# Optimization experiments

Hardware: AMD Instinct MI355X
Metric: run time of the kernel (lower is better)

## Reference

```python
import jax, jax.numpy as jnp
import numpy as np

D_MODEL = 1024
NUM_HEADS = 16
HEAD_DIM = D_MODEL // NUM_HEADS


def setup_inputs() -> dict:
    key = jax.random.key(0)
    ks = jax.random.split(key, 11)
    S, B, D = 2048, 2, D_MODEL
    scale = 1.0 / np.sqrt(D)
    inp = {
        'query': jax.random.normal(ks[0], (S, B, D), dtype=jnp.float32),
        'key': jax.random.normal(ks[1], (S, B, D), dtype=jnp.float32),
        'value': jax.random.normal(ks[2], (S, B, D), dtype=jnp.float32),
        'Wq': jax.random.normal(ks[3], (D, D), dtype=jnp.float32) * scale,
        'bq': jnp.zeros((D,), dtype=jnp.float32),
        'Wk': jax.random.normal(ks[4], (D, D), dtype=jnp.float32) * scale,
        'bk': jnp.zeros((D,), dtype=jnp.float32),
        'Wv': jax.random.normal(ks[5], (D, D), dtype=jnp.float32) * scale,
        'bv': jnp.zeros((D,), dtype=jnp.float32),
        'Wo': jax.random.normal(ks[6], (D, D), dtype=jnp.float32) * scale,
        'bo': jnp.zeros((D,), dtype=jnp.float32),
    }
    return inp


def reference(query, key, value, Wq, bq, Wk, bk, Wv, bv, Wo, bo):
    # query/key/value: [S, B, D] (seq-first, as in the torch module)
    S, B, D = query.shape
    H, Hd = NUM_HEADS, HEAD_DIM
    # Linear: x @ W.T + b (torch convention), then split heads -> [B, H, S, Hd]
    def proj_heads(x, W, b):
        y = jnp.einsum('sbd,ed->sbe', x, W) + b  # [S, B, D]
        return y.reshape(x.shape[0], B, H, Hd).transpose(1, 2, 0, 3)
    q = proj_heads(query, Wq, bq)   # [B, H, S, Hd]
    k = proj_heads(key, Wk, bk)     # [B, H, Sk, Hd]
    v = proj_heads(value, Wv, bv)   # [B, H, Sk, Hd]
    scores = jnp.einsum('bhsd,bhtd->bhst', q, k) / jnp.sqrt(jnp.asarray(Hd, q.dtype))
    probs = jax.nn.softmax(scores, axis=-1)  # dropout p=0.0 -> identity
    attn = jnp.einsum('bhst,bhtd->bhsd', probs, v)  # [B, H, S, Hd]
    attn = attn.transpose(2, 0, 1, 3).reshape(S, B, D)  # [S, B, D]
    out = jnp.einsum('sbd,ed->sbe', attn, Wo) + bo
    return out
```

## Files before the change

### kernel.cpp

```cpp
#include <hip/hip_runtime.h>
#include <stdint.h>

#define S_LEN 2048
#define BATCH 2
#define DM    1024
#define NH    16
#define HD    64
#define MROWS 4096

typedef float f32x4 __attribute__((ext_vector_type(4)));
typedef short bfrag __attribute__((ext_vector_type(8)));
typedef unsigned short u16x4_t __attribute__((ext_vector_type(4)));
typedef unsigned short u16x8_t __attribute__((ext_vector_type(8)));
typedef int i32x4_t __attribute__((ext_vector_type(4)));

#define EXP2F(x) __builtin_amdgcn_exp2f(x)

__device__ inline f32x4 mfma16(bfrag a, bfrag b, f32x4 c) {
    return __builtin_amdgcn_mfma_f32_16x16x32_bf16(a, b, c, 0, 0, 0);
}

__device__ inline unsigned short bf16_rn(float x) {
    unsigned u = __builtin_bit_cast(unsigned, x);
    return (unsigned short)((u + 0x7fffu + ((u >> 16) & 1u)) >> 16);
}

__device__ inline void split_bf16(float x, unsigned short &h, unsigned short &l) {
    unsigned u = __builtin_bit_cast(unsigned, x);
    h = (unsigned short)(u >> 16);
    float hf = __builtin_bit_cast(float, u & 0xffff0000u);
    float r = x - hf;
    l = (unsigned short)(__builtin_bit_cast(unsigned, r) >> 16);
}

__device__ inline unsigned pack_rhu(float a, float b) {
    unsigned ua = __builtin_bit_cast(unsigned, a) + 0x8000u;
    unsigned ub = __builtin_bit_cast(unsigned, b) + 0x8000u;
    return (ua >> 16) | (ub & 0xffff0000u);
}

typedef __attribute__((address_space(1))) const unsigned int as1_u32;
typedef __attribute__((address_space(3))) unsigned int as3_u32;
__device__ inline void async16(void* lds, const void* g) {
    __builtin_amdgcn_global_load_lds((as1_u32*)g, (as3_u32*)lds, 16, 0, 0);
}

__global__ __launch_bounds__(256)
void cvt_kernel(const float* __restrict__ Wq, const float* __restrict__ Wk,
                const float* __restrict__ Wv, const float* __restrict__ Wo,
                const float* __restrict__ Qin, const float* __restrict__ Kin,
                const float* __restrict__ Vin,
                unsigned short* __restrict__ Wqb, unsigned short* __restrict__ Wkb,
                unsigned short* __restrict__ Wvb,
                unsigned short* __restrict__ Woh, unsigned short* __restrict__ Wol,
                unsigned short* __restrict__ Qa,  unsigned short* __restrict__ Ka,
                unsigned short* __restrict__ Va)
{
    const int z = blockIdx.z;
    size_t idx = ((size_t)blockIdx.x * 256 + threadIdx.x) * 8;
    const size_t limit = (z < 4) ? (size_t)DM * DM : (size_t)MROWS * DM;
    if (idx >= limit) return;
    const float* src = (z == 0) ? Wq : (z == 1) ? Wk : (z == 2) ? Wv :
                       (z == 3) ? Wo : (z == 4) ? Qin : (z == 5) ? Kin : Vin;
    float4 f0 = *(const float4*)&src[idx];
    float4 f1 = *(const float4*)&src[idx + 4];
    if (z != 3) {
        unsigned short* dst = (z == 0) ? Wqb : (z == 1) ? Wkb : (z == 2) ? Wvb :
                              (z == 4) ? Qa  : (z == 5) ? Ka  : Va;
        u16x8_t v = { bf16_rn(f0.x), bf16_rn(f0.y), bf16_rn(f0.z), bf16_rn(f0.w),
                      bf16_rn(f1.x), bf16_rn(f1.y), bf16_rn(f1.z), bf16_rn(f1.w) };
        *(u16x8_t*)&dst[idx] = v;
    } else {
        unsigned short h0,h1,h2,h3,h4,h5,h6,h7, l0,l1,l2,l3,l4,l5,l6,l7;
        split_bf16(f0.x,h0,l0); split_bf16(f0.y,h1,l1);
        split_bf16(f0.z,h2,l2); split_bf16(f0.w,h3,l3);
        split_bf16(f1.x,h4,l4); split_bf16(f1.y,h5,l5);
        split_bf16(f1.z,h6,l6); split_bf16(f1.w,h7,l7);
        u16x8_t vh = {h0,h1,h2,h3,h4,h5,h6,h7};
        u16x8_t vl = {l0,l1,l2,l3,l4,l5,l6,l7};
        *(u16x8_t*)&Woh[idx] = vh;
        *(u16x8_t*)&Wol[idx] = vl;
    }
}

__global__ __launch_bounds__(256)
void qkv_gemm(const unsigned short* __restrict__ Qa,
              const unsigned short* __restrict__ Ka,
              const unsigned short* __restrict__ Va,
              const unsigned short* __restrict__ Wqb,
              const unsigned short* __restrict__ Wkb,
              const unsigned short* __restrict__ Wvb,
              const float* __restrict__ bq, const float* __restrict__ bk,
              const float* __restrict__ bv,
              unsigned short* __restrict__ Qb, unsigned short* __restrict__ Kb,
              unsigned short* __restrict__ Vt)
{
    __shared__ unsigned short sA[128*32];
    __shared__ unsigned short sB[128*32];

    const int tid = threadIdx.x, lane = tid & 63, w4 = tid >> 6;
    const int m16 = lane & 15, q4 = lane >> 4;
    const int wr = w4 >> 1, wc = w4 & 1;
    const int z = blockIdx.z;

    int id = blockIdx.x + 8 * blockIdx.y;
    int j  = id >> 3;
    const int m0 = ((id & 7) * 4 + (j & 3)) * 128;
    const int n0 = (j >> 2) * 128;

    const unsigned short* A = (z == 0) ? Qa : (z == 1) ? Ka : Va;
    const unsigned short* W = (z == 0) ? Wqb : (z == 1) ? Wkb : Wvb;
    const float* bias = (z == 0) ? bq : (z == 1) ? bk : bv;
    unsigned short* outp = (z == 0) ? Qb : (z == 1) ? Kb : Vt;

    const int G1 = tid + 256;
    const int r0 = tid >> 2, g0 = (tid & 3) ^ ((r0 ^ (r0 >> 2)) & 3);
    const int r1 = G1  >> 2, g1 = (G1  & 3) ^ ((r1 ^ (r1 >> 2)) & 3);
    const char* gA0 = (const char*)A + (size_t)(m0 + r0) * 2048 + g0 * 16;
    const char* gA1 = (const char*)A + (size_t)(m0 + r1) * 2048 + g1 * 16;
    const char* gB0 = (const char*)W + (size_t)(n0 + r0) * 2048 + g0 * 16;
    const char* gB1 = (const char*)W + (size_t)(n0 + r1) * 2048 + g1 * 16;
    char* ldsA0 = (char*)sA + w4 * 1024;
    char* ldsA1 = (char*)sA + 4096 + w4 * 1024;
    char* ldsB0 = (char*)sB + w4 * 1024;
    char* ldsB1 = (char*)sB + 4096 + w4 * 1024;

    int offA[4], offB[4];
    #pragma unroll
    for (int rt = 0; rt < 4; rt++) {
        int r = wr * 64 + rt * 16 + m16;
        offA[rt] = r * 32 + ((q4 ^ ((r ^ (r >> 2)) & 3)) << 3);
    }
    #pragma unroll
    for (int ct = 0; ct < 4; ct++) {
        int r = wc * 64 + ct * 16 + m16;
        offB[ct] = r * 32 + ((q4 ^ ((r ^ (r >> 2)) & 3)) << 3);
    }

    f32x4 acc[4][4];
    const f32x4 zero4 = {0.f, 0.f, 0.f, 0.f};
    #pragma unroll
    for (int i = 0; i < 4; i++)
        #pragma unroll
        for (int jj = 0; jj < 4; jj++) acc[i][jj] = zero4;

    for (int k0 = 0; k0 < DM; k0 += 32) {
        async16(ldsA0, gA0);
        async16(ldsA1, gA1);
        async16(ldsB0, gB0);
        async16(ldsB1, gB1);
        gA0 += 64; gA1 += 64; gB0 += 64; gB1 += 64;
        __syncthreads();

        bfrag a[4], bb[4];
        #pragma unroll
        for (int rt = 0; rt < 4; rt++) a[rt]  = *(const bfrag*)&sA[offA[rt]];
        #pragma unroll
        for (int ct = 0; ct < 4; ct++) bb[ct] = *(const bfrag*)&sB[offB[ct]];

        #pragma unroll
        for (int rt = 0; rt < 4; rt++)
            #pragma unroll
            for (int ct = 0; ct < 4; ct++)
                acc[rt][ct] = mfma16(a[rt], bb[ct], acc[rt][ct]);
        __syncthreads();
    }

    const float SCALE = (z == 0) ? 0.18033688011112042f : 1.0f;
    #pragma unroll
    for (int rt = 0; rt < 4; rt++)
        #pragma unroll
        for (int ct = 0; ct < 4; ct++)
            #pragma unroll
            for (int reg = 0; reg < 4; reg++) {
                int r = m0 + wr * 64 + rt * 16 + q4 * 4 + reg;
                int c = n0 + wc * 64 + ct * 16 + m16;
                float v = (acc[rt][ct][reg] + bias[c]) * SCALE;
                int s = r >> 1, b = r & 1, hh = c >> 6, d = c & 63;
                unsigned short bv16 = bf16_rn(v);
                if (z == 2)
                    outp[((size_t)(b * NH + hh) * HD + d) * S_LEN + s] = bv16;
                else
                    outp[((size_t)(b * NH + hh) * S_LEN + s) * HD + d] = bv16;
            }
}

__global__ __launch_bounds__(256)
void attn_kernel(const unsigned short* __restrict__ Qb,
                 const unsigned short* __restrict__ Kb,
                 const unsigned short* __restrict__ Vt,
                 unsigned short* __restrict__ Op,
                 float* __restrict__ Lp)
{
    __shared__ unsigned short sK[2][64*64];
    __shared__ unsigned short sV[2][64*64];
    __shared__ unsigned int   sPT[4][32*36];

    const int tid = threadIdx.x, lane = tid & 63, w4 = tid >> 6;
    const int m16 = lane & 15, q4 = lane >> 4;

    int id = blockIdx.x;
    int xcd = id & 7, j = id >> 3;
    const int bh   = xcd * 4 + (j >> 5);
    const int rem  = j & 31;
    const int half = rem & 1;
    const int qc   = rem >> 1;
    const int qw   = qc * 128 + w4 * 32;
    const int tbase = half * (S_LEN / 2);

    const unsigned short* Qp = Qb + (size_t)bh * (S_LEN * HD);
    const unsigned short* Kp = Kb + (size_t)bh * (S_LEN * HD);
    const unsigned short* Vp = Vt + (size_t)bh * (S_LEN * HD);
    unsigned int* pw = sPT[w4];

    bfrag aq[2][2];
    #pragma unroll
    for (int nt = 0; nt < 2; nt++)
        #pragma unroll
        for (int kc = 0; kc < 2; kc++)
            aq[nt][kc] = *(const bfrag*)&Qp[(size_t)(qw + nt*16 + m16) * HD + kc*32 + q4*8];

    const int r0 = tid >> 3,         g0 = (tid & 7) ^ (r0 & 7);
    const int r1 = (tid + 256) >> 3, g1 = (tid & 7) ^ (r1 & 7);
    const char* gK0 = (const char*)Kp + (size_t)(tbase + r0) * 128 + g0 * 16;
    const char* gK1 = (const char*)Kp + (size_t)(tbase + r1) * 128 + g1 * 16;
    const char* gV0 = (const char*)Vp + (size_t)r0 * 4096 + tbase * 2 + g0 * 16;
    const char* gV1 = (const char*)Vp + (size_t)r1 * 4096 + tbase * 2 + g1 * 16;
    const int ldsw = w4 * 1024;

    const f32x4 zero4 = {0.f, 0.f, 0.f, 0.f};
    f32x4 O[2][4];
    float lp[2] = {0.f, 0.f};
    #pragma unroll
    for (int nt = 0; nt < 2; nt++)
        #pragma unroll
        for (int dt = 0; dt < 4; dt++) O[nt][dt] = zero4;

    async16((char*)sK[0] + ldsw,        gK0);
    async16((char*)sK[0] + 4096 + ldsw, gK1);
    async16((char*)sV[0] + ldsw,        gV0);
    async16((char*)sV[0] + 4096 + ldsw, gV1);

    const int NT = (S_LEN / 2) / 64;
    for (int it = 0; it < NT; it++) {
        const int bi = it & 1;
        __syncthreads();
        if (it + 1 < NT) {
            size_t ko = (size_t)(it + 1) * 8192, vo = (size_t)(it + 1) * 128;
            async16((char*)sK[bi^1] + ldsw,        gK0 + ko);
            async16((char*)sK[bi^1] + 4096 + ldsw, gK1 + ko);
            async16((char*)sV[bi^1] + ldsw,        gV0 + vo);
            async16((char*)sV[bi^1] + 4096 + ldsw, gV1 + vo);
        }

        const unsigned short* kb = sK[bi];
        const unsigned short* vb = sV[bi];

        bfrag ak[4][2];
        #pragma unroll
        for (int mt = 0; mt < 4; mt++) {
            int r = mt*16 + m16, s = r & 7;
            ak[mt][0] = *(const bfrag*)&kb[r*64 + ((q4     ^ s) << 3)];
            ak[mt][1] = *(const bfrag*)&kb[r*64 + (((4+q4) ^ s) << 3)];
        }

        #pragma unroll
        for (int nt = 0; nt < 2; nt++) {
            f32x4 Sc[4];
            #pragma unroll
            for (int mt = 0; mt < 4; mt++) {
                Sc[mt] = mfma16(ak[mt][0], aq[nt][0], zero4);
                Sc[mt] = mfma16(ak[mt][1], aq[nt][1], Sc[mt]);
            }
            unsigned rowb = (unsigned)(nt*16 + m16) * 36;
            #pragma unroll
            for (int mt = 0; mt < 4; mt++) {
                float p0 = EXP2F(Sc[mt][0]), p1 = EXP2F(Sc[mt][1]);
                float p2 = EXP2F(Sc[mt][2]), p3 = EXP2F(Sc[mt][3]);
                lp[nt] += (p0 + p1) + (p2 + p3);
                uint2 c2 = { pack_rhu(p0, p1), pack_rhu(p2, p3) };
                *(uint2*)&pw[rowb + mt*8 + q4*2] = c2;
            }
        }

        bfrag av[4][2];
        #pragma unroll
        for (int dt = 0; dt < 4; dt++) {
            int r = dt*16 + m16, s = r & 7;
            av[dt][0] = *(const bfrag*)&vb[r*64 + ((q4     ^ s) << 3)];
            av[dt][1] = *(const bfrag*)&vb[r*64 + (((4+q4) ^ s) << 3)];
        }

        #pragma unroll
        for (int nt = 0; nt < 2; nt++) {
            bfrag bp[2];
            #pragma unroll
            for (int kc = 0; kc < 2; kc++)
                bp[kc] = __builtin_bit_cast(bfrag,
                    *(const i32x4_t*)&pw[(unsigned)(nt*16 + m16) * 36 + kc*16 + q4*4]);
            #pragma unroll
            for (int dt = 0; dt < 4; dt++) {
                O[nt][dt] = mfma16(av[dt][0], bp[0], O[nt][dt]);
                O[nt][dt] = mfma16(av[dt][1], bp[1], O[nt][dt]);
            }
        }
    }

    const size_t OPH = (size_t)BATCH * NH * S_LEN * HD;
    unsigned short* Ob = Op + (size_t)half * OPH;
    float* Lb = Lp + (size_t)half * (BATCH * NH * S_LEN);
    #pragma unroll
    for (int nt = 0; nt < 2; nt++) {
        float l = lp[nt];
        l += __shfl_xor(l, 16);
        l += __shfl_xor(l, 32);
        int q = qw + nt*16 + m16;
        if (q4 == 0) Lb[(size_t)bh * S_LEN + q] = l;
        size_t rb = ((size_t)bh * S_LEN + q) * HD;
        #pragma unroll
        for (int dt = 0; dt < 4; dt++) {
            u16x4_t o = { bf16_rn(O[nt][dt][0]), bf16_rn(O[nt][dt][1]),
                          bf16_rn(O[nt][dt][2]), bf16_rn(O[nt][dt][3]) };
            *(u16x4_t*)&Ob[rb + dt*16 + q4*4] = o;
        }
    }
}

__global__ __launch_bounds__(256)
void cmb_kernel(const unsigned short* __restrict__ Op,
                const float* __restrict__ Lp,
                unsigned short* __restrict__ Ap)
{
    const size_t OPH = (size_t)BATCH * NH * S_LEN * HD;
    int idx = blockIdx.x * 256 + threadIdx.x;
    int rho = idx >> 3, dg = idx & 7;
    size_t e = (size_t)rho * HD + dg * 8;
    float inv = 1.0f / (Lp[rho] + Lp[BATCH*NH*S_LEN + rho]);
    u16x8_t a = *(const u16x8_t*)&Op[e];
    u16x8_t b2 = *(const u16x8_t*)&Op[OPH + e];
    u16x8_t r;
    #pragma unroll
    for (int i = 0; i < 8; i++) {
        float fa = __builtin_bit_cast(float, (unsigned)(unsigned short)a[i]  << 16);
        float fb = __builtin_bit_cast(float, (unsigned)(unsigned short)b2[i] << 16);
        r[i] = bf16_rn((fa + fb) * inv);
    }
    int bh = rho >> 11, q = rho & 2047;
    int b = bh >> 4, h = bh & 15;
    *(u16x8_t*)&Ap[((size_t)(q * 2 + b)) * DM + h * 64 + dg * 8] = r;
}

__global__ __launch_bounds__(256)
void out_gemm(const unsigned short* __restrict__ Ap,
              const unsigned short* __restrict__ Woh,
              const unsigned short* __restrict__ Wol,
              const float* __restrict__ bo, float* __restrict__ out)
{
    __shared__ unsigned short sA[128*32];
    __shared__ unsigned short sH[64*32];
    __shared__ unsigned short sL[64*32];

    const int tid = threadIdx.x, lane = tid & 63, w4 = tid >> 6;
    const int m16 = lane & 15, q4 = lane >> 4;
    const int wr = w4 >> 1, wc = w4 & 1;

    int id = blockIdx.x + 16 * blockIdx.y;
    int j  = id >> 3;
    const int m0 = ((id & 7) * 4 + (j & 3)) * 128;
    const int n0 = (j >> 2) * 64;

    const int G1 = tid + 256;
    const int r0 = tid >> 2, g0 = (tid & 3) ^ ((r0 ^ (r0 >> 2)) & 3);
    const int r1 = G1  >> 2, g1 = (G1  & 3) ^ ((r1 ^ (r1 >> 2)) & 3);
    const char* gA0 = (const char*)Ap  + (size_t)(m0 + r0) * 2048 + g0 * 16;
    const char* gA1 = (const char*)Ap  + (size_t)(m0 + r1) * 2048 + g1 * 16;
    const char* gH  = (const char*)Woh + (size_t)(n0 + r0) * 2048 + g0 * 16;
    const char* gL  = (const char*)Wol + (size_t)(n0 + r0) * 2048 + g0 * 16;
    char* ldsA0 = (char*)sA + w4 * 1024;
    char* ldsA1 = (char*)sA + 4096 + w4 * 1024;
    char* ldsH  = (char*)sH + w4 * 1024;
    char* ldsL  = (char*)sL + w4 * 1024;

    int offA[4], offB[2];
    #pragma unroll
    for (int rt = 0; rt < 4; rt++) {
        int r = wr * 64 + rt * 16 + m16;
        offA[rt] = r * 32 + ((q4 ^ ((r ^ (r >> 2)) & 3)) << 3);
    }
    #pragma unroll
    for (int ct = 0; ct < 2; ct++) {
        int r = wc * 32 + ct * 16 + m16;
        offB[ct] = r * 32 + ((q4 ^ ((r ^ (r >> 2)) & 3)) << 3);
    }

    f32x4 acc[4][2];
    const f32x4 zero4 = {0.f, 0.f, 0.f, 0.f};
    #pragma unroll
    for (int i = 0; i < 4; i++)
        #pragma unroll
        for (int jj = 0; jj < 2; jj++) acc[i][jj] = zero4;

    for (int k0 = 0; k0 < DM; k0 += 32) {
        async16(ldsA0, gA0);
        async16(ldsA1, gA1);
        async16(ldsH,  gH);
        async16(ldsL,  gL);
        gA0 += 64; gA1 += 64; gH += 64; gL += 64;
        __syncthreads();

        bfrag a[4], bh2[2], bl2[2];
        #pragma unroll
        for (int rt = 0; rt < 4; rt++) a[rt] = *(const bfrag*)&sA[offA[rt]];
        #pragma unroll
        for (int ct = 0; ct < 2; ct++) {
            bh2[ct] = *(const bfrag*)&sH[offB[ct]];
            bl2[ct] = *(const bfrag*)&sL[offB[ct]];
        }
        #pragma unroll
        for (int rt = 0; rt < 4; rt++)
            #pragma unroll
            for (int ct = 0; ct < 2; ct++) {
                acc[rt][ct] = mfma16(a[rt], bh2[ct], acc[rt][ct]);
                acc[rt][ct] = mfma16(a[rt], bl2[ct], acc[rt][ct]);
            }
        __syncthreads();
    }

    #pragma unroll
    for (int rt = 0; rt < 4; rt++)
        #pragma unroll
        for (int ct = 0; ct < 2; ct++)
            #pragma unroll
            for (int reg = 0; reg < 4; reg++) {
                int r = m0 + wr * 64 + rt * 16 + q4 * 4 + reg;
                int c = n0 + wc * 32 + ct * 16 + m16;
                out[(size_t)r * DM + c] = acc[rt][ct][reg] + bo[c];
            }
}

extern "C" void kernel_launch(void* const* d_in, const int* in_sizes, int n_in,
                              void* d_out, int out_size, void* d_ws, size_t ws_size,
                              hipStream_t stream)
{
    const float* query = (const float*)d_in[0];
    const float* key   = (const float*)d_in[1];
    const float* value = (const float*)d_in[2];
    const float* Wq    = (const float*)d_in[3];
    const float* bq    = (const float*)d_in[4];
    const float* Wk    = (const float*)d_in[5];
    const float* bk    = (const float*)d_in[6];
    const float* Wv    = (const float*)d_in[7];
    const float* bv    = (const float*)d_in[8];
    const float* Wo    = (const float*)d_in[9];
    const float* bo    = (const float*)d_in[10];

    char* ws = (char*)d_ws;
    const size_t MB = 1u << 20;
    unsigned short* Qb  = (unsigned short*)(ws);
    unsigned short* Kb  = (unsigned short*)(ws +  8*MB);
    unsigned short* Vt  = (unsigned short*)(ws + 16*MB);
    unsigned short* Woh = (unsigned short*)(ws + 24*MB);
    unsigned short* Wol = (unsigned short*)(ws + 26*MB);
    unsigned short* Wqb = (unsigned short*)(ws + 28*MB);
    unsigned short* Wkb = (unsigned short*)(ws + 30*MB);
    unsigned short* Wvb = (unsigned short*)(ws + 32*MB);
    unsigned short* Va  = (unsigned short*)(ws + 34*MB);
    float*          Lp  = (float*)         (ws + 28*MB);
    unsigned short* Apl = (unsigned short*)(ws + 34*MB);
    unsigned short* Opart = (unsigned short*)d_out;
    unsigned short* Qa  = (unsigned short*)d_out;
    unsigned short* Ka  = (unsigned short*)d_out + (size_t)MROWS*DM;

    cvt_kernel<<<dim3(2048, 1, 7), 256, 0, stream>>>(
        Wq, Wk, Wv, Wo, query, key, value,
        Wqb, Wkb, Wvb, Woh, Wol, Qa, Ka, Va);
    qkv_gemm<<<dim3(8, 32, 3), 256, 0, stream>>>(
        Qa, Ka, Va, Wqb, Wkb, Wvb, bq, bk, bv, Qb, Kb, Vt);
    attn_kernel<<<dim3(1024), 256, 0, stream>>>(Qb, Kb, Vt, Opart, Lp);
    cmb_kernel<<<dim3(2048), 256, 0, stream>>>(Opart, Lp, Apl);
    out_gemm<<<dim3(16, 32), 256, 0, stream>>>(Apl, Woh, Wol, bo, (float*)d_out);
}
```

Measured before the change: 241.6 us.

## Keep attention probabilities in registers via permlane swaps instead of LDS round-trip

The softmax probability tile is no longer written to shared memory and re-read as the B operand of the PV MFMA. Instead it is converted with the hardware packed bf16 convert and rearranged across lanes with permlane32/permlane16 swap instructions to form the MFMA fragment directly. This removes the per-iteration LDS stores and loads plus the per-wave scratch buffer, which also frees shared memory. Launch bounds now request 4 blocks per CU. Rounding changes from round-half-up to round-to-nearest-even, and correctness depends on the lane permutation matching the expected fragment layout.

Measured after the change: 228.4 us. 5.4% less time.

```diff
diff --git a/kernel.cpp b/kernel.cpp
--- a/kernel.cpp
+++ b/kernel.cpp
@@ -33,10 +33,17 @@
     l = (unsigned short)(__builtin_bit_cast(unsigned, r) >> 16);
 }
 
-__device__ inline unsigned pack_rhu(float a, float b) {
-    unsigned ua = __builtin_bit_cast(unsigned, a) + 0x8000u;
-    unsigned ub = __builtin_bit_cast(unsigned, b) + 0x8000u;
-    return (ua >> 16) | (ub & 0xffff0000u);
+__device__ inline unsigned cvtpk_bf16(float lo, float hi) {
+    unsigned r;
+    asm("v_cvt_pk_bf16_f32 %0, %1, %2" : "=v"(r) : "v"(lo), "v"(hi));
+    return r;
+}
+
+__device__ inline void pl32swap(unsigned &a, unsigned &b) {
+    asm("v_permlane32_swap_b32 %0, %1" : "+v"(a), "+v"(b));
+}
+__device__ inline void pl16swap(unsigned &a, unsigned &b) {
+    asm("v_permlane16_swap_b32 %0, %1" : "+v"(a), "+v"(b));
 }
 
 typedef __attribute__((address_space(1))) const unsigned int as1_u32;
@@ -185,7 +192,7 @@
             }
 }
 
-__global__ __launch_bounds__(256)
+__global__ __launch_bounds__(256, 4)
 void attn_kernel(const unsigned short* __restrict__ Qb,
                  const unsigned short* __restrict__ Kb,
                  const unsigned short* __restrict__ Vt,
@@ -194,7 +201,6 @@
 {
     __shared__ unsigned short sK[2][64*64];
     __shared__ unsigned short sV[2][64*64];
-    __shared__ unsigned int   sPT[4][32*36];
 
     const int tid = threadIdx.x, lane = tid & 63, w4 = tid >> 6;
     const int m16 = lane & 15, q4 = lane >> 4;
@@ -211,7 +217,6 @@
     const unsigned short* Qp = Qb + (size_t)bh * (S_LEN * HD);
     const unsigned short* Kp = Kb + (size_t)bh * (S_LEN * HD);
     const unsigned short* Vp = Vt + (size_t)bh * (S_LEN * HD);
-    unsigned int* pw = sPT[w4];
 
     bfrag aq[2][2];
     #pragma unroll
@@ -264,6 +269,7 @@
             ak[mt][1] = *(const bfrag*)&kb[r*64 + (((4+q4) ^ s) << 3)];
         }
 
+        bfrag bpv[2][2];
         #pragma unroll
         for (int nt = 0; nt < 2; nt++) {
             f32x4 Sc[4];
@@ -272,14 +278,25 @@
                 Sc[mt] = mfma16(ak[mt][0], aq[nt][0], zero4);
                 Sc[mt] = mfma16(ak[mt][1], aq[nt][1], Sc[mt]);
             }
-            unsigned rowb = (unsigned)(nt*16 + m16) * 36;
+            unsigned u0[4], u1[4];
             #pragma unroll
             for (int mt = 0; mt < 4; mt++) {
                 float p0 = EXP2F(Sc[mt][0]), p1 = EXP2F(Sc[mt][1]);
                 float p2 = EXP2F(Sc[mt][2]), p3 = EXP2F(Sc[mt][3]);
                 lp[nt] += (p0 + p1) + (p2 + p3);
-                uint2 c2 = { pack_rhu(p0, p1), pack_rhu(p2, p3) };
-                *(uint2*)&pw[rowb + mt*8 + q4*2] = c2;
+                u0[mt] = cvtpk_bf16(p0, p1);
+                u1[mt] = cvtpk_bf16(p2, p3);
+            }
+            #pragma unroll
+            for (int kc = 0; kc < 2; kc++) {
+                unsigned a0 = u0[2*kc], b0 = u0[2*kc+1];
+                pl32swap(a0, b0);
+                pl16swap(a0, b0);
+                unsigned a1 = u1[2*kc], b1 = u1[2*kc+1];
+                pl32swap(a1, b1);
+                pl16swap(a1, b1);
+                i32x4_t w = { (int)a0, (int)a1, (int)b0, (int)b1 };
+                bpv[nt][kc] = __builtin_bit_cast(bfrag, w);
             }
         }
 
@@ -292,18 +309,12 @@
         }
 
         #pragma unroll
-        for (int nt = 0; nt < 2; nt++) {
-            bfrag bp[2];
-            #pragma unroll
-            for (int kc = 0; kc < 2; kc++)
-                bp[kc] = __builtin_bit_cast(bfrag,
-                    *(const i32x4_t*)&pw[(unsigned)(nt*16 + m16) * 36 + kc*16 + q4*4]);
+        for (int nt = 0; nt < 2; nt++)
             #pragma unroll
             for (int dt = 0; dt < 4; dt++) {
-                O[nt][dt] = mfma16(av[dt][0], bp[0], O[nt][dt]);
-                O[nt][dt] = mfma16(av[dt][1], bp[1], O[nt][dt]);
-            }
-        }
+                O[nt][dt] = mfma16(av[dt][0], bpv[nt][0], O[nt][dt]);
+                O[nt][dt] = mfma16(av[dt][1], bpv[nt][1], O[nt][dt]);
+            }
     }
 
     const size_t OPH = (size_t)BATCH * NH * S_LEN * HD;
```
